# Kernel tuning notes

Hardware: AMD Instinct MI355X
Metric: run time of the kernel (lower is better)

Reference implementation:

```python
import jax, jax.numpy as jnp
import numpy as np

H, NH, KVH = 2048, 16, 4
HD = H // NH            # 128
GROUPS = NH // KVH      # 4
E, TOPK = 8, 2
I_MOE, I_SH = 1408, 5632
THETA = 1000000.0
EPS = 1e-6
B, S = 1, 1024


def rms_norm(x, w):
    var = jnp.mean(jnp.square(x), axis=-1, keepdims=True)
    return x * jax.lax.rsqrt(var + EPS) * w


def rotate_half(x):
    x1, x2 = jnp.split(x, 2, axis=-1)
    return jnp.concatenate([-x2, x1], axis=-1)


def apply_rope(q, k, position_ids):
    # q: [B,S,NH,HD], k: [B,S,KVH,HD]
    inv_freq = 1.0 / (THETA ** (jnp.arange(0, HD, 2, dtype=jnp.float32) / HD))
    ang = position_ids.astype(jnp.float32)[..., None] * inv_freq  # [B,S,HD/2]
    emb = jnp.concatenate([ang, ang], axis=-1)                    # [B,S,HD]
    cos = jnp.cos(emb)[:, :, None, :]
    sin = jnp.sin(emb)[:, :, None, :]
    q = q * cos + rotate_half(q) * sin
    k = k * cos + rotate_half(k) * sin
    return q, k


def setup_inputs() -> dict:
    key = jax.random.key(0)
    ks = jax.random.split(key, 24)
    sd = 0.02
    inp = {
        "hidden_states": jax.random.normal(ks[0], (B, S, H), jnp.float32),
        "position_ids": jnp.arange(S, dtype=jnp.int32)[None, :].repeat(B, 0),
        "ln1_w": jnp.ones((H,), jnp.float32),
        "ln2_w": jnp.ones((H,), jnp.float32),
        "q_w": jax.random.normal(ks[1], (H, NH * HD), jnp.float32) * sd,
        "q_b": jnp.zeros((NH * HD,), jnp.float32),
        "k_w": jax.random.normal(ks[2], (H, KVH * HD), jnp.float32) * sd,
        "k_b": jnp.zeros((KVH * HD,), jnp.float32),
        "v_w": jax.random.normal(ks[3], (H, KVH * HD), jnp.float32) * sd,
        "v_b": jnp.zeros((KVH * HD,), jnp.float32),
        "o_w": jax.random.normal(ks[4], (NH * HD, H), jnp.float32) * sd,
        "router_w": jax.random.normal(ks[5], (H, E), jnp.float32) * sd,
        "e_gate": jax.random.normal(ks[6], (E, H, I_MOE), jnp.float32) * sd,
        "e_up": jax.random.normal(ks[7], (E, H, I_MOE), jnp.float32) * sd,
        "e_down": jax.random.normal(ks[8], (E, I_MOE, H), jnp.float32) * sd,
        "s_gate": jax.random.normal(ks[9], (H, I_SH), jnp.float32) * sd,
        "s_up": jax.random.normal(ks[10], (H, I_SH), jnp.float32) * sd,
        "s_down": jax.random.normal(ks[11], (I_SH, H), jnp.float32) * sd,
        "sg_w": jax.random.normal(ks[12], (H, 1), jnp.float32) * sd,
    }
    return inp


def attention(x, position_ids, q_w, q_b, k_w, k_b, v_w, v_b, o_w):
    b, s, _ = x.shape
    q = (x @ q_w + q_b).reshape(b, s, NH, HD)
    k = (x @ k_w + k_b).reshape(b, s, KVH, HD)
    v = (x @ v_w + v_b).reshape(b, s, KVH, HD)
    q, k = apply_rope(q, k, position_ids)
    # GQA: repeat kv heads
    k = jnp.repeat(k, GROUPS, axis=2)  # [b,s,NH,HD]
    v = jnp.repeat(v, GROUPS, axis=2)
    scale = HD ** -0.5
    scores = jnp.einsum("bqhd,bkhd->bhqk", q, k) * scale
    causal = jnp.tril(jnp.ones((s, s), bool))
    scores = jnp.where(causal[None, None], scores, jnp.finfo(scores.dtype).min)
    probs = jax.nn.softmax(scores, axis=-1)
    out = jnp.einsum("bhqk,bkhd->bqhd", probs, v).reshape(b, s, NH * HD)
    return out @ o_w


def sparse_moe(x, router_w, e_gate, e_up, e_down, s_gate, s_up, s_down, sg_w):
    b, s, h = x.shape
    xf = x.reshape(b * s, h)  # [T,H]
    T = b * s
    probs = jax.nn.softmax(xf @ router_w, axis=-1)        # [T,E]
    top_w, top_i = jax.lax.top_k(probs, TOPK)             # norm_topk_prob=False
    weights = jnp.zeros((T, E), xf.dtype).at[jnp.arange(T)[:, None], top_i].set(top_w)
    g = jax.nn.silu(jnp.einsum("th,ehi->eti", xf, e_gate))
    u = jnp.einsum("th,ehi->eti", xf, e_up)
    d = jnp.einsum("eti,eih->eth", g * u, e_down)         # [E,T,H]
    moe_out = jnp.einsum("eth,te->th", d, weights)
    shared = (jax.nn.silu(xf @ s_gate) * (xf @ s_up)) @ s_down
    shared = shared * jax.nn.sigmoid(xf @ sg_w)
    return (moe_out + shared).reshape(b, s, h)


def reference(hidden_states, position_ids, ln1_w, ln2_w, q_w, q_b, k_w, k_b,
              v_w, v_b, o_w, router_w, e_gate, e_up, e_down,
              s_gate, s_up, s_down, sg_w):
    h = hidden_states
    attn = attention(rms_norm(h, ln1_w), position_ids,
                     q_w, q_b, k_w, k_b, v_w, v_b, o_w)
    h = h + attn
    moe = sparse_moe(rms_norm(h, ln2_w), router_w, e_gate, e_up, e_down,
                     s_gate, s_up, s_down, sg_w)
    return h + moe
```

## Files before the change

### kernel.cpp

```cpp
#include <hip/hip_runtime.h>
#include <hip/hip_bf16.h>

#define S_ 1024
#define H_ 2048
#define NH_ 16
#define KVH_ 4
#define HD_ 128
#define IM_ 1408
#define ISH_ 5632
#define E_ 8

typedef __bf16 bf16x8 __attribute__((ext_vector_type(8)));
typedef float f32x4 __attribute__((ext_vector_type(4)));

typedef unsigned int __attribute__((address_space(1))) as1_u32;
typedef unsigned int __attribute__((address_space(3))) as3_u32;

__device__ __forceinline__ void gload16(const void* g, void* l) {
  __builtin_amdgcn_global_load_lds((const as1_u32*)g, (as3_u32*)l, 16, 0, 0);
}

__device__ __forceinline__ short f2bf(float f) {
  unsigned u = __float_as_uint(f);
  u = u + 0x7FFFu + ((u >> 16) & 1u);
  return (short)(u >> 16);
}

__device__ __forceinline__ f32x4 mfma16(bf16x8 a, bf16x8 b, f32x4 c) {
  return __builtin_amdgcn_mfma_f32_16x16x32_bf16(a, b, c, 0, 0, 0);
}

template<bool MAXOP>
__device__ __forceinline__ float block_reduce(float v, float* sbuf) {
  #pragma unroll
  for (int o = 32; o >= 1; o >>= 1) {
    float t = __shfl_down(v, o);
    v = MAXOP ? fmaxf(v, t) : (v + t);
  }
  int lane = threadIdx.x & 63, w = threadIdx.x >> 6;
  if (lane == 0) sbuf[w] = v;
  __syncthreads();
  float r = sbuf[0];
  #pragma unroll
  for (int i = 1; i < 4; i++) r = MAXOP ? fmaxf(r, sbuf[i]) : (r + sbuf[i]);
  __syncthreads();
  return r;
}

struct TransDesc {
  const float* src; short* dst;
  int R, C, tx, perz, base;
  long long srcZ, dstZ;
};
struct TransAll { TransDesc d[10]; };

__global__ __launch_bounds__(256) void trans_all_k(TransAll ta) {
  __shared__ short tile[64][72];
  int bid = blockIdx.x;
  int w = 0;
  #pragma unroll
  for (int i = 1; i < 10; i++) if (bid >= ta.d[i].base) w = i;
  const TransDesc& D = ta.d[w];
  int local = bid - D.base;
  int z = local / D.perz, rem = local - z * D.perz;
  int by = rem / D.tx, bx = rem - by * D.tx;
  const float* src = D.src + (long long)z * D.srcZ;
  short* dst = D.dst + (long long)z * D.dstZ;
  const int r0 = by * 64, c0 = bx * 64;
  const int C = D.C, R = D.R;
  const int t = threadIdx.x;
  const int tr = t >> 4, tc4 = (t & 15) * 4;
  #pragma unroll
  for (int i = 0; i < 4; i++) {
    int r = tr + i * 16;
    float4 v = *(const float4*)&src[(size_t)(r0 + r) * C + c0 + tc4];
    tile[tc4 + 0][r] = f2bf(v.x);
    tile[tc4 + 1][r] = f2bf(v.y);
    tile[tc4 + 2][r] = f2bf(v.z);
    tile[tc4 + 3][r] = f2bf(v.w);
  }
  __syncthreads();
  const int row = t >> 2, kc = (t & 3) * 16;
  #pragma unroll
  for (int j = 0; j < 2; j++) {
    int kcol = kc + j * 8;
    *(int4*)&dst[(size_t)(c0 + row) * R + r0 + kcol] = *(const int4*)&tile[row][kcol];
  }
}

struct GemmP {
  const short* A; long long strideA; int adiv; int lda;
  const short* B; long long strideB; int bdiv; int ldb;
  void* C; long long strideC; int cdiv; int ldc;
  const int* e_off; const int* e_cnt;
  const int* list; const float* scale;
  float alpha;
  int M, N, K;
  int cskip, ckb;
  int ksplit, kchunk;
  int upoff;
};

template<int EPI>
__device__ __forceinline__ void gemm_body(const GemmP& p, int bx, int by, int bz,
                                          short* As, short* Bs) {
  constexpr bool FUSED = (EPI == 6 || EPI == 7);
  constexpr bool GATH  = (EPI == 7);
  constexpr int BM = 128, BN = 128, BK = 32;
  const int zo = bz / p.ksplit;
  const int kc = bz - zo * p.ksplit;
  const int m0 = by * BM;
  const int n0 = bx * (FUSED ? 64 : BN);
  if (FUSED && n0 >= p.N) return;

  int off = 0, cnt = p.M;
  if constexpr (EPI == 4 || GATH) {
    off = p.e_off[zo]; cnt = p.e_cnt[zo];
    if (m0 >= cnt) return;
  }
  if (p.cskip && n0 >= m0 + BM) return;
  int kend = p.ckb ? min(m0 + BM, p.K) : p.K;
  const int kbeg = kc * p.kchunk;
  kend = min(kend, kbeg + p.kchunk);
  if (kbeg >= kend) return;

  const short* Ab = p.A + (long long)(zo / p.adiv) * p.strideA;
  const short* Bb = p.B + (long long)(zo / p.bdiv) * p.strideB;

  const int tid = threadIdx.x;
  const int lane = tid & 63, wid = tid >> 6;
  const int wr = wid >> 1, wc = wid & 1;
  const int kg = lane >> 4, li = lane & 15;

  const int srow = tid >> 2;
  const int scol = (((tid & 3) ^ ((tid >> 3) & 3))) * 8;
  const short* aSrc[2];
  const short* bSrc[2];
  #pragma unroll
  for (int c = 0; c < 2; c++) {
    int ra = srow + c * 64;
    int gr;
    if constexpr (GATH)          { int rr = m0 + ra; if (rr >= cnt) rr = cnt - 1; gr = p.list[off + rr]; }
    else if constexpr (EPI == 4) { int rr = m0 + ra; if (rr >= cnt) rr = cnt - 1; gr = off + rr; }
    else                         gr = m0 + ra;
    aSrc[c] = Ab + (long long)gr * p.lda + scol;
    int br = FUSED ? (n0 + srow + (c ? p.upoff : 0)) : (n0 + srow + c * 64);
    bSrc[c] = Bb + (long long)br * p.ldb + scol;
  }

  f32x4 acc[4][4];
  #pragma unroll
  for (int i = 0; i < 4; i++)
    #pragma unroll
    for (int j = 0; j < 4; j++) acc[i][j] = (f32x4){0.f, 0.f, 0.f, 0.f};

  #pragma unroll
  for (int c = 0; c < 2; c++) {
    gload16(aSrc[c] + kbeg, &As[tid * 8 + c * 2048]);
    gload16(bSrc[c] + kbeg, &Bs[tid * 8 + c * 2048]);
  }
  __syncthreads();

  const int kgx = kg ^ ((li >> 1) & 3);
  int brow[4];
  #pragma unroll
  for (int nj = 0; nj < 4; nj++)
    brow[nj] = FUSED ? (((nj & 2) ? 64 : 0) + wc * 32 + (nj & 1) * 16 + li)
                     : (wc * 64 + nj * 16 + li);

  int cur = 0;
  for (int k0 = kbeg; k0 < kend; k0 += BK) {
    const int nk = k0 + BK;
    if (nk < kend) {
      #pragma unroll
      for (int c = 0; c < 2; c++) {
        gload16(aSrc[c] + nk, &As[(cur ^ 1) * 4096 + tid * 8 + c * 2048]);
        gload16(bSrc[c] + nk, &Bs[(cur ^ 1) * 4096 + tid * 8 + c * 2048]);
      }
    }
    bf16x8 av[4], bv[4];
    #pragma unroll
    for (int mi = 0; mi < 4; mi++)
      av[mi] = *(const bf16x8*)&As[cur * 4096 + (wr * 64 + mi * 16 + li) * BK + kgx * 8];
    #pragma unroll
    for (int nj = 0; nj < 4; nj++)
      bv[nj] = *(const bf16x8*)&Bs[cur * 4096 + brow[nj] * BK + kgx * 8];
    #pragma unroll
    for (int mi = 0; mi < 4; mi++)
      #pragma unroll
      for (int nj = 0; nj < 4; nj++)
        acc[mi][nj] = mfma16(av[mi], bv[nj], acc[mi][nj]);
    __syncthreads();
    cur ^= 1;
  }

  const long long zc = (long long)(zo / p.cdiv) * p.strideC;
  if constexpr (FUSED) {
    short* C = (short*)p.C;
    #pragma unroll
    for (int mi = 0; mi < 4; mi++) {
      #pragma unroll
      for (int nj = 0; nj < 2; nj++) {
        #pragma unroll
        for (int r = 0; r < 4; r++) {
          int ml = wr * 64 + mi * 16 + kg * 4 + r;
          int mg = m0 + ml;
          int ng = n0 + wc * 32 + nj * 16 + li;
          float g = acc[mi][nj][r], u = acc[mi][nj + 2][r];
          float gu = g * (1.f / (1.f + __expf(-g))) * u;
          if constexpr (GATH) {
            if (mg < cnt) C[(long long)(off + mg) * p.ldc + ng] = f2bf(gu);
          } else {
            C[(long long)mg * p.ldc + ng] = f2bf(gu);
          }
        }
      }
    }
  } else {
    #pragma unroll
    for (int mi = 0; mi < 4; mi++) {
      #pragma unroll
      for (int nj = 0; nj < 4; nj++) {
        #pragma unroll
        for (int r = 0; r < 4; r++) {
          int ml = wr * 64 + mi * 16 + kg * 4 + r;
          int nl2 = wc * 64 + nj * 16 + li;
          int mg = m0 + ml, ng = n0 + nl2;
          float v = acc[mi][nj][r] * p.alpha;
          if constexpr (EPI == 0) {
            float* C = (float*)p.C + zc;
            __builtin_nontemporal_store(v, &C[(long long)mg * p.ldc + ng]);
          } else if constexpr (EPI == 1) {
            float* C = (float*)p.C + zc;
            atomicAdd(&C[(long long)mg * p.ldc + ng], v);
          } else if constexpr (EPI == 4) {
            if (mg < cnt) {
              float* C = (float*)p.C;
              int tok = p.list[off + mg];
              atomicAdd(&C[(long long)tok * p.ldc + ng], p.scale[off + mg] * v);
            }
          } else if constexpr (EPI == 5) {
            float* C = (float*)p.C;
            atomicAdd(&C[(long long)mg * p.ldc + ng], p.scale[mg] * v);
          }
        }
      }
    }
  }
}

template<int EPI>
__global__ __launch_bounds__(256) void gemm_bt(GemmP p) {
  __shared__ __align__(16) short As[2 * 128 * 32];
  __shared__ __align__(16) short Bs[2 * 128 * 32];
  gemm_body<EPI>(p, blockIdx.x, blockIdx.y, blockIdx.z, As, Bs);
}

__global__ __launch_bounds__(256) void gemm_gu_dual(GemmP pe, GemmP ps) {
  __shared__ __align__(16) short As[2 * 128 * 32];
  __shared__ __align__(16) short Bs[2 * 128 * 32];
  int z = blockIdx.z;
  if (z < E_) gemm_body<7>(pe, blockIdx.x, blockIdx.y, z, As, Bs);
  else        gemm_body<6>(ps, (z - E_) * 22 + blockIdx.x, blockIdx.y, 0, As, Bs);
}

template<int EPI1, int EPI2>
__global__ __launch_bounds__(256) void gemm_dual(GemmP p1, GemmP p2, int z1) {
  __shared__ __align__(16) short As[2 * 128 * 32];
  __shared__ __align__(16) short Bs[2 * 128 * 32];
  int z = blockIdx.z;
  if (z < z1) gemm_body<EPI1>(p1, blockIdx.x, blockIdx.y, z, As, Bs);
  else        gemm_body<EPI2>(p2, blockIdx.x, blockIdx.y, z - z1, As, Bs);
}

__global__ __launch_bounds__(256) void prep_k(const int* pos_ids, float* ct, float* st,
                                              const float* qb, const float* kb, const float* vb,
                                              float* qkv, float* attn_f, int* counts) {
  int bid = blockIdx.x, tid = threadIdx.x;
  if (bid == 0 && tid < 16) counts[tid] = 0;
  if (bid < 256) {
    int i = bid * 256 + tid;
    int p = i >> 6, f = i & 63;
    float pos = (float)pos_ids[p];
    float inv = powf(1.0e6f, -(float)f * (1.f / 64.f));
    float a = pos * inv;
    ct[i] = cosf(a); st[i] = sinf(a);
  } else if (bid < 3328) {
    int idx = (bid - 256) * 256 + tid;
    int j = (idx * 4) % 3072;
    float4 v;
    const float* b = (j < 2048) ? qb + j : ((j < 2560) ? kb + (j - 2048) : vb + (j - 2560));
    v.x = b[0]; v.y = b[1]; v.z = b[2]; v.w = b[3];
    ((float4*)qkv)[idx] = v;
  } else {
    int idx = (bid - 3328) * 256 + tid;
    ((float4*)attn_f)[idx] = (float4){0.f, 0.f, 0.f, 0.f};
  }
}

__global__ __launch_bounds__(256) void rmsnorm_k(const float* x, const float* w, short* o,
                                                 float* copy_out, float* rs_out) {
  __shared__ float sbuf[4];
  int t = blockIdx.x;
  const float* xr = x + (long long)t * H_;
  float ss = 0.f;
  for (int i = threadIdx.x; i < H_ / 4; i += 256) {
    float4 v = ((const float4*)xr)[i];
    ss += v.x * v.x + v.y * v.y + v.z * v.z + v.w * v.w;
  }
  ss = block_reduce<false>(ss, sbuf);
  float rs = rsqrtf(ss * (1.f / (float)H_) + 1e-6f);
  for (int i = threadIdx.x; i < H_; i += 256) {
    float xv = xr[i];
    o[(long long)t * H_ + i] = f2bf(xv * rs * w[i]);
    if (copy_out) copy_out[(long long)t * H_ + i] = xv;
  }
  if (rs_out && threadIdx.x == 0) rs_out[t] = rs;
}

__global__ __launch_bounds__(256) void rope_fused_k(const float* qkv, short* qr, short* kr,
                                                    short* vt, const float* ct, const float* st) {
  int i = blockIdx.x * 256 + threadIdx.x;
  if (i < 2097152) {
    int t = i >> 11, j = i & 2047;
    int d = j & 127, f = d & 63;
    float c = ct[t * 64 + f], s = st[t * 64 + f];
    const float* row = qkv + (long long)t * 3072;
    float xv = row[j];
    float ov = (d < 64) ? -row[j + 64] : row[j - 64];
    qr[i] = f2bf(xv * c + ov * s);
  } else if (i < 2621440) {
    int j = i - 2097152;
    int t = j >> 9, jj = j & 511;
    int d = jj & 127, f = d & 63;
    float c = ct[t * 64 + f], s = st[t * 64 + f];
    const float* row = qkv + (long long)t * 3072 + 2048;
    float xv = row[jj];
    float ov = (d < 64) ? -row[jj + 64] : row[jj - 64];
    kr[j] = f2bf(xv * c + ov * s);
  } else {
    int j = i - 2621440;
    int kvh = j >> 17, rem = j & 131071;
    int d = rem >> 10, s_ = rem & 1023;
    vt[j] = f2bf(qkv[(long long)s_ * 3072 + 2560 + kvh * 128 + d]);
  }
}

__global__ __launch_bounds__(256) void cvt_bf16_k(const float* src, short* dst, int total) {
  int i = blockIdx.x * 256 + threadIdx.x;
  if (i < total) dst[i] = f2bf(src[i]);
}

__global__ __launch_bounds__(256) void softmax_k(const float* sc, short* P) {
  __shared__ float sbuf[4];
  long long row = blockIdx.x;
  int q = (int)(row & (S_ - 1));
  const float* sr = sc + row * S_;
  short* pr = P + row * S_;
  int L = q + 1;
  int Lcap = (q & ~127) + 128;
  float mx = -3.4e38f;
  for (int i = threadIdx.x; i < L; i += 256) mx = fmaxf(mx, sr[i]);
  mx = block_reduce<true>(mx, sbuf);
  float s = 0.f;
  for (int i = threadIdx.x; i < L; i += 256) s += __expf(sr[i] - mx);
  s = block_reduce<false>(s, sbuf);
  float inv = 1.f / s;
  for (int i = threadIdx.x; i < Lcap; i += 256) {
    float pv = (i < L) ? __expf(sr[i] - mx) * inv : 0.f;
    pr[i] = f2bf(pv);
  }
}

__global__ void router_k(const float* h2, const float* rs, const float* w2,
                         const float* rw, const float* sgw,
                         int* top_i, float* top_w, float* sg_sig, int* counts) {
  int t = blockIdx.x;
  int l = threadIdx.x;
  float le[8] = {0, 0, 0, 0, 0, 0, 0, 0};
  float ls = 0.f;
  float r = rs[t];
  for (int k = l; k < H_; k += 64) {
    float xv = h2[(long long)t * H_ + k] * r * w2[k];
    ls += xv * sgw[k];
    const float* rk = rw + k * E_;
    #pragma unroll
    for (int e = 0; e < E_; e++) le[e] += xv * rk[e];
  }
  #pragma unroll
  for (int o = 32; o >= 1; o >>= 1) {
    ls += __shfl_down(ls, o);
    #pragma unroll
    for (int e = 0; e < E_; e++) le[e] += __shfl_down(le[e], o);
  }
  if (l == 0) {
    float m = le[0];
    for (int e = 1; e < E_; e++) m = fmaxf(m, le[e]);
    float pe[8], s = 0.f;
    for (int e = 0; e < E_; e++) { pe[e] = __expf(le[e] - m); s += pe[e]; }
    float inv = 1.f / s;
    for (int e = 0; e < E_; e++) pe[e] *= inv;
    int i1 = 0;
    for (int e = 1; e < E_; e++) if (pe[e] > pe[i1]) i1 = e;
    int i2 = -1;
    for (int e = 0; e < E_; e++) if (e != i1 && (i2 < 0 || pe[e] > pe[i2])) i2 = e;
    top_i[2 * t] = i1; top_i[2 * t + 1] = i2;
    top_w[2 * t] = pe[i1]; top_w[2 * t + 1] = pe[i2];
    sg_sig[t] = 1.f / (1.f + __expf(-ls));
    atomicAdd(&counts[i1], 1); atomicAdd(&counts[i2], 1);
  }
}

__global__ void scan_k(const int* counts, int* offs) {
  if (threadIdx.x == 0 && blockIdx.x == 0) {
    int s = 0;
    for (int e = 0; e < E_; e++) { offs[e] = s; s += counts[e]; }
  }
}

__global__ __launch_bounds__(256) void fill_k(const int* top_i, const float* top_w, const int* offs,
                                              int* pos, int* list, float* pw) {
  int t = blockIdx.x * 256 + threadIdx.x;
  if (t >= S_) return;
  for (int j = 0; j < 2; j++) {
    int e = top_i[2 * t + j];
    int p_ = atomicAdd(&pos[e], 1);
    int slot = offs[e] + p_;
    list[slot] = t; pw[slot] = top_w[2 * t + j];
  }
}

static GemmP mkp() {
  GemmP p{};
  p.adiv = 1; p.bdiv = 1; p.cdiv = 1; p.alpha = 1.f;
  p.ksplit = 1; p.kchunk = 1 << 30;
  p.upoff = 0;
  return p;
}

extern "C" void kernel_launch(void* const* d_in, const int* in_sizes, int n_in,
                              void* d_out, int out_size, void* d_ws, size_t ws_size,
                              hipStream_t stream) {
  const float* hidden   = (const float*)d_in[0];
  const int*   pos_ids  = (const int*)d_in[1];
  const float* ln1_w    = (const float*)d_in[2];
  const float* ln2_w    = (const float*)d_in[3];
  const float* q_w      = (const float*)d_in[4];
  const float* q_b      = (const float*)d_in[5];
  const float* k_w      = (const float*)d_in[6];
  const float* k_b      = (const float*)d_in[7];
  const float* v_w      = (const float*)d_in[8];
  const float* v_b      = (const float*)d_in[9];
  const float* o_w      = (const float*)d_in[10];
  const float* router_w = (const float*)d_in[11];
  const float* e_gate   = (const float*)d_in[12];
  const float* e_up     = (const float*)d_in[13];
  const float* e_down   = (const float*)d_in[14];
  const float* s_gate   = (const float*)d_in[15];
  const float* s_up     = (const float*)d_in[16];
  const float* s_down   = (const float*)d_in[17];
  const float* sg_w     = (const float*)d_in[18];
  float* out = (float*)d_out;

  char* base = (char*)d_ws;
  size_t off_ = 0;
  auto alc = [&](size_t nbytes) -> char* {
    off_ = (off_ + 255) & ~(size_t)255;
    char* p = base + off_;
    off_ += nbytes;
    return p;
  };
  short* qkvT = (short*)alc((size_t)3072 * H_ * 2);
  short* oT   = (short*)alc((size_t)H_ * H_ * 2);
  short* eguT = (short*)alc((size_t)E_ * 2816 * H_ * 2);
  short* edT  = (short*)alc((size_t)E_ * H_ * IM_ * 2);
  short* sguT = (short*)alc((size_t)11264 * H_ * 2);
  short* sdT  = (short*)alc((size_t)H_ * ISH_ * 2);
  short* x1      = (short*)alc((size_t)S_ * H_ * 2);
  float* qkv_f   = (float*)alc((size_t)S_ * 3072 * 4);
  float* ct      = (float*)alc((size_t)S_ * 64 * 4);
  float* st      = (float*)alc((size_t)S_ * 64 * 4);
  short* qr      = (short*)alc((size_t)S_ * H_ * 2);
  short* kr      = (short*)alc((size_t)S_ * 512 * 2);
  short* vt      = (short*)alc((size_t)S_ * 512 * 2);
  float* attn_f  = (float*)alc((size_t)S_ * H_ * 4);
  short* attn    = (short*)alc((size_t)S_ * H_ * 2);
  float* h2      = (float*)alc((size_t)S_ * H_ * 4);
  short* x2      = (short*)alc((size_t)S_ * H_ * 2);
  float* rs2     = (float*)alc(S_ * 4);
  int*   top_i   = (int*)alc(2 * S_ * 4);
  float* top_w   = (float*)alc(2 * S_ * 4);
  float* sg_sig  = (float*)alc(S_ * 4);
  int*   counts  = (int*)alc(64);
  int*   pos     = counts + 8;
  int*   offs    = (int*)alc(32);
  int*   list    = (int*)alc(2 * S_ * 4);
  float* pw      = (float*)alc(2 * S_ * 4);
  char*  region  = alc(100663296);
  float* scores  = (float*)region;
  short* P       = (short*)(region + 67108864);
  short* gu_moeB = (short*)region;
  short* gushB   = (short*)(region + 16777216);

  {
    TransAll ta{};
    int b = 0;
    auto add = [&](int i, const float* s, short* d, int R, int C, int tz,
                   long long sZ, long long dZ) {
      int tx = C / 64, ty = R / 64;
      ta.d[i] = TransDesc{s, d, R, C, tx, tx * ty, b, sZ, dZ};
      b += tx * ty * tz;
    };
    add(0, q_w, qkvT, H_, H_, 1, 0, 0);
    add(1, k_w, qkvT + (size_t)2048 * H_, H_, 512, 1, 0, 0);
    add(2, v_w, qkvT + (size_t)2560 * H_, H_, 512, 1, 0, 0);
    add(3, o_w, oT, H_, H_, 1, 0, 0);
    add(4, e_gate, eguT, H_, IM_, E_, (long long)H_ * IM_, (long long)2816 * H_);
    add(5, e_up, eguT + (size_t)1408 * H_, H_, IM_, E_, (long long)H_ * IM_, (long long)2816 * H_);
    add(6, e_down, edT, IM_, H_, E_, (long long)IM_ * H_, (long long)IM_ * H_);
    add(7, s_gate, sguT, H_, ISH_, 1, 0, 0);
    add(8, s_up, sguT + (size_t)5632 * H_, H_, ISH_, 1, 0, 0);
    add(9, s_down, sdT, ISH_, H_, 1, 0, 0);
    trans_all_k<<<b, 256, 0, stream>>>(ta);
  }

  prep_k<<<5376, 256, 0, stream>>>(pos_ids, ct, st, q_b, k_b, v_b, qkv_f, attn_f, counts);
  rmsnorm_k<<<S_, 256, 0, stream>>>(hidden, ln1_w, x1, h2, nullptr);

  {
    GemmP p = mkp();
    p.A = x1; p.lda = H_;
    p.B = qkvT; p.ldb = H_;
    p.C = qkv_f; p.ldc = 3072;
    p.M = S_; p.N = 3072; p.K = H_;
    p.ksplit = 2; p.kchunk = 1024;
    gemm_bt<1><<<dim3(24, 8, 2), 256, 0, stream>>>(p);
  }

  rope_fused_k<<<12288, 256, 0, stream>>>(qkv_f, qr, kr, vt, ct, st);

  {
    GemmP p = mkp();
    p.A = qr; p.strideA = HD_; p.lda = H_;
    p.B = kr; p.strideB = HD_; p.bdiv = 4; p.ldb = 512;
    p.C = scores; p.strideC = (long long)S_ * S_; p.ldc = S_;
    p.alpha = 0.08838834764831845f;
    p.M = S_; p.N = S_; p.K = HD_; p.cskip = 1;
    p.kchunk = HD_;
    gemm_bt<0><<<dim3(8, 8, NH_), 256, 0, stream>>>(p);
  }
  softmax_k<<<NH_ * S_, 256, 0, stream>>>(scores, P);
  {
    GemmP p = mkp();
    p.A = P; p.strideA = (long long)S_ * S_; p.lda = S_;
    p.B = vt; p.strideB = (long long)HD_ * S_; p.bdiv = 4; p.ldb = S_;
    p.C = attn_f; p.strideC = HD_; p.ldc = H_;
    p.M = S_; p.N = HD_; p.K = S_; p.ckb = 1;
    p.ksplit = 4; p.kchunk = 256;
    gemm_bt<1><<<dim3(1, 8, NH_ * 4), 256, 0, stream>>>(p);
  }
  cvt_bf16_k<<<8192, 256, 0, stream>>>(attn_f, attn, S_ * H_);
  {
    GemmP p = mkp();
    p.A = attn; p.lda = H_;
    p.B = oT; p.ldb = H_;
    p.C = h2; p.ldc = H_;
    p.M = S_; p.N = H_; p.K = H_;
    p.ksplit = 4; p.kchunk = 512;
    gemm_bt<1><<<dim3(16, 8, 4), 256, 0, stream>>>(p);
  }

  rmsnorm_k<<<S_, 256, 0, stream>>>(h2, ln2_w, x2, out, rs2);

  router_k<<<S_, 64, 0, stream>>>(h2, rs2, ln2_w, router_w, sg_w, top_i, top_w, sg_sig, counts);
  scan_k<<<1, 1, 0, stream>>>(counts, offs);
  fill_k<<<4, 256, 0, stream>>>(top_i, top_w, offs, pos, list, pw);

  {
    GemmP pe = mkp();
    pe.A = x2; pe.lda = H_;
    pe.B = eguT; pe.strideB = (long long)2816 * H_; pe.ldb = H_;
    pe.C = gu_moeB; pe.ldc = IM_;
    pe.e_off = offs; pe.e_cnt = counts; pe.list = list;
    pe.M = S_; pe.N = IM_; pe.K = H_;
    pe.upoff = IM_;
    GemmP ps = mkp();
    ps.A = x2; ps.lda = H_;
    ps.B = sguT; ps.ldb = H_;
    ps.C = gushB; ps.ldc = ISH_;
    ps.M = S_; ps.N = ISH_; ps.K = H_;
    ps.upoff = ISH_;
    gemm_gu_dual<<<dim3(22, 8, 12), 256, 0, stream>>>(pe, ps);
  }

  {
    GemmP pe = mkp();
    pe.A = gu_moeB; pe.lda = IM_;
    pe.B = edT; pe.strideB = (long long)H_ * IM_; pe.ldb = IM_;
    pe.C = out; pe.ldc = H_;
    pe.e_off = offs; pe.e_cnt = counts; pe.list = list; pe.scale = pw;
    pe.M = S_; pe.N = H_; pe.K = IM_;
    pe.ksplit = 2; pe.kchunk = 704;
    GemmP ps = mkp();
    ps.A = gushB; ps.lda = ISH_;
    ps.B = sdT; ps.ldb = ISH_;
    ps.C = out; ps.ldc = H_; ps.scale = sg_sig;
    ps.M = S_; ps.N = H_; ps.K = ISH_;
    ps.ksplit = 4; ps.kchunk = 1408;
    gemm_dual<4, 5><<<dim3(16, 8, E_ * 2 + 4), 256, 0, stream>>>(pe, ps, E_ * 2);
  }
}
```

Baseline: 610.7 us.

## Fuse weight transpose, prep and first RMSNorm into one launch; raise QKV split-K

```diff
diff --git a/kernel.cpp b/kernel.cpp
--- a/kernel.cpp
+++ b/kernel.cpp
@@ -54,37 +54,81 @@
 };
 struct TransAll { TransDesc d[10]; };
 
-__global__ __launch_bounds__(256) void trans_all_k(TransAll ta) {
-  __shared__ short tile[64][72];
-  int bid = blockIdx.x;
-  int w = 0;
-  #pragma unroll
-  for (int i = 1; i < 10; i++) if (bid >= ta.d[i].base) w = i;
-  const TransDesc& D = ta.d[w];
-  int local = bid - D.base;
-  int z = local / D.perz, rem = local - z * D.perz;
-  int by = rem / D.tx, bx = rem - by * D.tx;
-  const float* src = D.src + (long long)z * D.srcZ;
-  short* dst = D.dst + (long long)z * D.dstZ;
-  const int r0 = by * 64, c0 = bx * 64;
-  const int C = D.C, R = D.R;
+__global__ __launch_bounds__(256) void mega_k(TransAll ta, int transBlocks,
+                                              const int* pos_ids, float* ct, float* st,
+                                              const float* qb, const float* kb, const float* vb,
+                                              float* qkv, float* attn_f, int* counts,
+                                              const float* hidden, const float* ln1_w,
+                                              short* x1, float* h2) {
+  __shared__ float tile[64][68];
+  __shared__ float sbuf[4];
+  const int bid = blockIdx.x;
   const int t = threadIdx.x;
-  const int tr = t >> 4, tc4 = (t & 15) * 4;
-  #pragma unroll
-  for (int i = 0; i < 4; i++) {
-    int r = tr + i * 16;
-    float4 v = *(const float4*)&src[(size_t)(r0 + r) * C + c0 + tc4];
-    tile[tc4 + 0][r] = f2bf(v.x);
-    tile[tc4 + 1][r] = f2bf(v.y);
-    tile[tc4 + 2][r] = f2bf(v.z);
-    tile[tc4 + 3][r] = f2bf(v.w);
-  }
-  __syncthreads();
-  const int row = t >> 2, kc = (t & 3) * 16;
-  #pragma unroll
-  for (int j = 0; j < 2; j++) {
-    int kcol = kc + j * 8;
-    *(int4*)&dst[(size_t)(c0 + row) * R + r0 + kcol] = *(const int4*)&tile[row][kcol];
+  if (bid < transBlocks) {
+    int w = 0;
+    #pragma unroll
+    for (int i = 1; i < 10; i++) if (bid >= ta.d[i].base) w = i;
+    const TransDesc& D = ta.d[w];
+    int local = bid - D.base;
+    int z = local / D.perz, rem = local - z * D.perz;
+    int by = rem / D.tx, bx = rem - by * D.tx;
+    const float* src = D.src + (long long)z * D.srcZ;
+    short* dst = D.dst + (long long)z * D.dstZ;
+    const int r0 = by * 64, c0 = bx * 64;
+    const int C = D.C, R = D.R;
+    #pragma unroll
+    for (int i = 0; i < 4; i++) {
+      int idx = t + i * 256;
+      int row = idx >> 4, c4 = (idx & 15) * 4;
+      f32x4 v = __builtin_nontemporal_load(
+          (const f32x4*)&src[(size_t)(r0 + row) * C + c0 + c4]);
+      *(f32x4*)&tile[row][c4] = v;
+    }
+    __syncthreads();
+    const int col = t >> 2, seg = t & 3;
+    short outv[16];
+    #pragma unroll
+    for (int j = 0; j < 16; j++)
+      outv[j] = f2bf(tile[seg * 16 + j][col]);
+    short* dp = &dst[(size_t)(c0 + col) * R + r0 + seg * 16];
+    *(int4*)dp = *(const int4*)&outv[0];
+    *(int4*)(dp + 8) = *(const int4*)&outv[8];
+  } else if (bid < transBlocks + 5376) {
+    int pb = bid - transBlocks;
+    if (pb == 0 && t < 16) counts[t] = 0;
+    if (pb < 256) {
+      int i = pb * 256 + t;
+      int p = i >> 6, f = i & 63;
+      float pos = (float)pos_ids[p];
+      float inv = powf(1.0e6f, -(float)f * (1.f / 64.f));
+      float a = pos * inv;
+      ct[i] = cosf(a); st[i] = sinf(a);
+    } else if (pb < 3328) {
+      int idx = (pb - 256) * 256 + t;
+      int j = (idx * 4) % 3072;
+      float4 v;
+      const float* b = (j < 2048) ? qb + j : ((j < 2560) ? kb + (j - 2048) : vb + (j - 2560));
+      v.x = b[0]; v.y = b[1]; v.z = b[2]; v.w = b[3];
+      ((float4*)qkv)[idx] = v;
+    } else {
+      int idx = (pb - 3328) * 256 + t;
+      ((float4*)attn_f)[idx] = (float4){0.f, 0.f, 0.f, 0.f};
+    }
+  } else {
+    int tr = bid - transBlocks - 5376;
+    const float* xr = hidden + (long long)tr * H_;
+    float ss = 0.f;
+    for (int i = t; i < H_ / 4; i += 256) {
+      float4 v = ((const float4*)xr)[i];
+      ss += v.x * v.x + v.y * v.y + v.z * v.z + v.w * v.w;
+    }
+    ss = block_reduce<false>(ss, sbuf);
+    float rs = rsqrtf(ss * (1.f / (float)H_) + 1e-6f);
+    for (int i = t; i < H_; i += 256) {
+      float xv = xr[i];
+      x1[(long long)tr * H_ + i] = f2bf(xv * rs * ln1_w[i]);
+      h2[(long long)tr * H_ + i] = xv;
+    }
   }
 }
 
@@ -271,31 +315,6 @@
   int z = blockIdx.z;
   if (z < z1) gemm_body<EPI1>(p1, blockIdx.x, blockIdx.y, z, As, Bs);
   else        gemm_body<EPI2>(p2, blockIdx.x, blockIdx.y, z - z1, As, Bs);
-}
-
-__global__ __launch_bounds__(256) void prep_k(const int* pos_ids, float* ct, float* st,
-                                              const float* qb, const float* kb, const float* vb,
-                                              float* qkv, float* attn_f, int* counts) {
-  int bid = blockIdx.x, tid = threadIdx.x;
-  if (bid == 0 && tid < 16) counts[tid] = 0;
-  if (bid < 256) {
-    int i = bid * 256 + tid;
-    int p = i >> 6, f = i & 63;
-    float pos = (float)pos_ids[p];
-    float inv = powf(1.0e6f, -(float)f * (1.f / 64.f));
-    float a = pos * inv;
-    ct[i] = cosf(a); st[i] = sinf(a);
-  } else if (bid < 3328) {
-    int idx = (bid - 256) * 256 + tid;
-    int j = (idx * 4) % 3072;
-    float4 v;
-    const float* b = (j < 2048) ? qb + j : ((j < 2560) ? kb + (j - 2048) : vb + (j - 2560));
-    v.x = b[0]; v.y = b[1]; v.z = b[2]; v.w = b[3];
-    ((float4*)qkv)[idx] = v;
-  } else {
-    int idx = (bid - 3328) * 256 + tid;
-    ((float4*)attn_f)[idx] = (float4){0.f, 0.f, 0.f, 0.f};
-  }
 }
 
 __global__ __launch_bounds__(256) void rmsnorm_k(const float* x, const float* w, short* o,
@@ -521,11 +540,10 @@
     add(7, s_gate, sguT, H_, ISH_, 1, 0, 0);
     add(8, s_up, sguT + (size_t)5632 * H_, H_, ISH_, 1, 0, 0);
     add(9, s_down, sdT, ISH_, H_, 1, 0, 0);
-    trans_all_k<<<b, 256, 0, stream>>>(ta);
-  }
-
-  prep_k<<<5376, 256, 0, stream>>>(pos_ids, ct, st, q_b, k_b, v_b, qkv_f, attn_f, counts);
-  rmsnorm_k<<<S_, 256, 0, stream>>>(hidden, ln1_w, x1, h2, nullptr);
+    mega_k<<<b + 5376 + 1024, 256, 0, stream>>>(ta, b, pos_ids, ct, st, q_b, k_b, v_b,
+                                                qkv_f, attn_f, counts,
+                                                hidden, ln1_w, x1, h2);
+  }
 
   {
     GemmP p = mkp();
@@ -533,8 +551,8 @@
     p.B = qkvT; p.ldb = H_;
     p.C = qkv_f; p.ldc = 3072;
     p.M = S_; p.N = 3072; p.K = H_;
-    p.ksplit = 2; p.kchunk = 1024;
-    gemm_bt<1><<<dim3(24, 8, 2), 256, 0, stream>>>(p);
+    p.ksplit = 4; p.kchunk = 512;
+    gemm_bt<1><<<dim3(24, 8, 4), 256, 0, stream>>>(p);
   }
 
   rope_fused_k<<<12288, 256, 0, stream>>>(qkv_f, qr, kr, vt, ct, st);
```

New measurement: 610.4 us. Within noise of the previous version (-0.1%).
